# Optimization experiments

Measured on AMD Instinct MI355X. Metric: run time of the kernel, lower is better.

Reference implementation:

```python
import jax, jax.numpy as jnp
import numpy as np

B, N1, N2, F = 128, 100, 2000, 128
NC = N1 + N2
T = 10
L0, L1, L2 = 32, 32, 16


def setup_inputs() -> dict:
    key = jax.random.key(0)
    ks = jax.random.split(key, 16)
    atom_types = jnp.array([1, 6, 7, 8, 9, 11, 12, 15, 16, 17], dtype=jnp.int32)
    # per-type MLP params, stacked over type dim T (matches build():
    # stddev 1/sqrt(layer_size) for hidden layers, 0.01 for output, zero biases)
    inp = {
        "frag1_layer": jax.random.normal(ks[0], (B, N1, F), jnp.float32),
        "frag2_layer": jax.random.normal(ks[1], (B, N2, F), jnp.float32),
        "complex_layer": jax.random.normal(ks[2], (B, NC, F), jnp.float32),
        "frag1_z": jax.random.randint(ks[3], (B, N1), 0, 18, jnp.int32),
        "frag2_z": jax.random.randint(ks[4], (B, N2), 0, 18, jnp.int32),
        "complex_z": jax.random.randint(ks[5], (B, NC), 0, 18, jnp.int32),
        "type_w0": jax.random.normal(ks[6], (T, F, L0), jnp.float32) * (1.0 / np.sqrt(L0)),
        "type_b0": jnp.zeros((T, L0), jnp.float32),
        "type_w1": jax.random.normal(ks[7], (T, L0, L1), jnp.float32) * (1.0 / np.sqrt(L1)),
        "type_b1": jnp.zeros((T, L1), jnp.float32),
        "type_w2": jax.random.normal(ks[8], (T, L1, L2), jnp.float32) * (1.0 / np.sqrt(L2)),
        "type_b2": jnp.zeros((T, L2), jnp.float32),
        "out_w": jax.random.normal(ks[9], (T, L2, 1), jnp.float32) * 0.01,
        "out_b": jnp.zeros((T, 1), jnp.float32),
        "atom_types": atom_types,
    }
    return inp


def reference(frag1_layer, frag2_layer, complex_layer, frag1_z, frag2_z, complex_z,
              type_w0, type_b0, type_w1, type_b1, type_w2, type_b2,
              out_w, out_b, atom_types):
    def per_type_energy(x, z):
        # dense compute for ALL atom types, then mask-route (same math as original)
        h = jax.nn.relu(jnp.einsum('bnf,tfh->tbnh', x, type_w0) + type_b0[:, None, None, :])
        h = jax.nn.relu(jnp.einsum('tbnh,thk->tbnk', h, type_w1) + type_b1[:, None, None, :])
        h = jax.nn.relu(jnp.einsum('tbnk,tkm->tbnm', h, type_w2) + type_b2[:, None, None, :])
        o = jnp.einsum('tbnm,tmo->tbno', h, out_w)[..., 0] + out_b[:, None, None, 0]  # [T,B,N]
        mask = z[None, :, :] == atom_types[:, None, None]  # [T,B,N]
        per_atom = jnp.sum(jnp.where(mask, o, jnp.zeros_like(o)), axis=0)  # [B,N]
        return jnp.sum(per_atom, axis=1)  # [B]

    e1 = per_type_energy(frag1_layer, frag1_z)
    e2 = per_type_energy(frag2_layer, frag2_z)
    ec = per_type_energy(complex_layer, complex_z)
    binding = ec - (e1 + e2)
    return binding[:, None]  # [B,1]
```

## Files before the change

kernel.cpp:

```cpp
#include <hip/hip_runtime.h>

#define B_ 128
#define N1_ 100
#define N2_ 2000
#define NC_ 2100
#define F_ 128
#define NT_ 10
#define L0_ 32
#define L1_ 32
#define L2_ 16

#define NA1 (B_*N1_)
#define NA2 (B_*N2_)
#define NAC (B_*NC_)
#define NATOT (NA1+NA2+NAC)
#define NBUCK (NT_*B_)
#define CAP_B 512
#define NFILL (NATOT/256)

#define WT_STRIDEH 11520

#define WS_CURSORS 0
#define WS_WPACK   8192
#define WS_LISTS   (WS_WPACK + NT_*WT_STRIDEH*2)
#define WS_NEEDED  ((size_t)WS_LISTS + (size_t)NBUCK*CAP_B*4)

typedef short bf16x8 __attribute__((ext_vector_type(8)));
typedef float f32x4 __attribute__((ext_vector_type(4)));

#define MFMA(a,b,c) __builtin_amdgcn_mfma_f32_16x16x32_bf16((a),(b),(c),0,0,0)

__device__ __forceinline__ unsigned short f2bf(float f){
  unsigned u = __float_as_uint(f);
  unsigned r = (u + 0x7FFFu + ((u >> 16) & 1u)) >> 16;
  return (unsigned short)r;
}
__device__ __forceinline__ float bf2f(unsigned short h){
  return __uint_as_float(((unsigned)h) << 16);
}

__device__ __forceinline__ void cvt8u(uint4 a, uint4 b, bf16x8& hi, bf16x8& lo){
  unsigned u[8] = {a.x, a.y, a.z, a.w, b.x, b.y, b.z, b.w};
  union { bf16x8 v; unsigned uu[4]; } H, L;
  #pragma unroll
  for (int i = 0; i < 4; ++i){
    unsigned p = u[2*i], qq = u[2*i+1];
    H.uu[i] = __builtin_amdgcn_perm(qq, p, 0x07060302u);
    unsigned ra = __float_as_uint(__uint_as_float(p)  - __uint_as_float(p  & 0xFFFF0000u));
    unsigned rb = __float_as_uint(__uint_as_float(qq) - __uint_as_float(qq & 0xFFFF0000u));
    L.uu[i] = __builtin_amdgcn_perm(rb, ra, 0x07060302u);
  }
  hi = H.v; lo = L.v;
}

__device__ __forceinline__ unsigned packsplit(float h){
  unsigned uh = __float_as_uint(h);
  unsigned tr = uh & 0xFFFF0000u;
  float res = h - __uint_as_float(tr);
  return tr | (__float_as_uint(res) >> 16);
}

__device__ __forceinline__ void unpack8(uint4 p0, uint4 p1, bf16x8& hi, bf16x8& lo){
  unsigned pp[8] = {p0.x, p0.y, p0.z, p0.w, p1.x, p1.y, p1.z, p1.w};
  union { bf16x8 v; unsigned uu[4]; } H, L;
  #pragma unroll
  for (int i = 0; i < 4; ++i){
    H.uu[i] = __builtin_amdgcn_perm(pp[2*i+1], pp[2*i], 0x07060302u);
    L.uu[i] = __builtin_amdgcn_perm(pp[2*i+1], pp[2*i], 0x05040100u);
  }
  hi = H.v; lo = L.v;
}

__device__ __forceinline__ void decode_atom(int g,
    const int* __restrict__ z1, const int* __restrict__ z2, const int* __restrict__ zc,
    int& tensor, int& row, int& b, int& z){
  if (g < NA1){ tensor = 0; row = g; b = g / N1_; z = z1[g]; }
  else if (g < NA1 + NA2){ int i = g - NA1; tensor = 1; row = i; b = i / N2_; z = z2[i]; }
  else { int i = g - NA1 - NA2; tensor = 2; row = i; b = i / NC_; z = zc[i]; }
}


__global__ __launch_bounds__(256) void k_fillprep(
    const int* __restrict__ z1, const int* __restrict__ z2, const int* __restrict__ zc,
    const int* __restrict__ atypes,
    const float* __restrict__ tw0, const float* __restrict__ tb0,
    const float* __restrict__ tw1, const float* __restrict__ tb1,
    const float* __restrict__ tw2, const float* __restrict__ tb2,
    const float* __restrict__ ow, const float* __restrict__ ob,
    unsigned* __restrict__ cursors, unsigned* __restrict__ lists,
    unsigned short* __restrict__ wpack, float* __restrict__ out){
  int tid = threadIdx.x;
  if (blockIdx.x >= NFILL){
    int t = blockIdx.x - NFILL;
    unsigned short* base = wpack + (size_t)t * WT_STRIDEH;
    const float* w0 = tw0 + (size_t)t * (F_ * L0_);
    for (int i = tid; i < 4096; i += 256){
      int ks = i >> 10, rem = i & 1023;
      int nt = rem >> 9, rem2 = rem & 511;
      int lane = rem2 >> 3, e = rem2 & 7;
      float f = w0[(ks * 32 + (lane >> 4) * 8 + e) * L0_ + nt * 16 + (lane & 15)];
      unsigned short hi = f2bf(f);
      unsigned short lo = f2bf(f - bf2f(hi));
      int off = (ks * 2 + nt) * 1024 + lane * 8 + e;
      base[off] = hi;
      base[off + 512] = lo;
    }
    const float* w1 = tw1 + (size_t)t * (L0_ * L1_);
    for (int i = tid; i < 1024; i += 256){
      int nt = i >> 9, rem2 = i & 511;
      int lane = rem2 >> 3, e = rem2 & 7;
      float f = w1[((lane >> 4) * 8 + e) * L1_ + nt * 16 + (lane & 15)];
      unsigned short hi = f2bf(f);
      unsigned short lo = f2bf(f - bf2f(hi));
      int off = 8192 + nt * 1024 + lane * 8 + e;
      base[off] = hi;
      base[off + 512] = lo;
    }
    const float* w2 = tw2 + (size_t)t * (L1_ * L2_);
    for (int i = tid; i < 512; i += 256){
      int lane = i >> 3, e = i & 7;
      float f = w2[((lane >> 4) * 8 + e) * L2_ + (lane & 15)];
      unsigned short hi = f2bf(f);
      unsigned short lo = f2bf(f - bf2f(hi));
      int off = 10240 + lane * 8 + e;
      base[off] = hi;
      base[off + 512] = lo;
    }
    float* prm = (float*)(base + 11264);
    if (tid < 32) prm[tid] = tb0[t * L0_ + tid];
    else if (tid < 64) prm[tid] = tb1[t * L1_ + tid - 32];
    else if (tid < 80) prm[tid] = tb2[t * L2_ + tid - 64];
    else if (tid < 96) prm[tid] = ow[t * L2_ + tid - 80];
    else if (tid == 96) prm[96] = ob[t];
    if (t == 0 && tid >= 128 && tid < 128 + B_) out[tid - 128] = 0.0f;
    return;
  }
  __shared__ int lut[32];
  __shared__ unsigned lhist[NBUCK];
  __shared__ unsigned lbase[NBUCK];
  for (int i = tid; i < NBUCK; i += 256) lhist[i] = 0u;
  if (tid < 32) lut[tid] = -1;
  __syncthreads();
  if (tid < NT_) lut[atypes[tid] & 31] = tid;
  __syncthreads();
  int g = blockIdx.x * 256 + tid;
  int bucket = -1; unsigned entv = 0u;
  {
    int tensor, row, b, z;
    decode_atom(g, z1, z2, zc, tensor, row, b, z);
    int t = lut[z & 31];
    if (t >= 0){
      bucket = t * B_ + b;
      entv = (unsigned)row | ((unsigned)tensor << 19);
      atomicAdd(&lhist[bucket], 1u);
    }
  }
  __syncthreads();
  for (int i = tid; i < NBUCK; i += 256){
    unsigned c = lhist[i];
    lbase[i] = c ? atomicAdd(&cursors[i], c) : 0u;
    lhist[i] = 0u;
  }
  __syncthreads();
  if (bucket >= 0){
    unsigned rank = atomicAdd(&lhist[bucket], 1u) + lbase[bucket];
    if (rank < CAP_B) lists[(size_t)bucket * CAP_B + rank] = entv;
  }
}


__global__ __launch_bounds__(64, 2) void k_main(
    const float* __restrict__ f1, const float* __restrict__ f2, const float* __restrict__ fc,
    const unsigned short* __restrict__ wpack,
    const unsigned* __restrict__ cursors, const unsigned* __restrict__ lists,
    float* __restrict__ out){
  int bucket = blockIdx.y;
  int count = (int)cursors[bucket];
  if (count > CAP_B) count = CAP_B;
  int quarter = (count + 3) >> 2;
  int lstart = blockIdx.x * quarter;
  int lend = lstart + quarter; if (lend > count) lend = count;
  int mycount = lend - lstart;
  if (mycount <= 0) return;
  int t = bucket >> 7, b = bucket & 127;
  int lane = threadIdx.x, q = lane >> 4, r16 = lane & 15;

  const unsigned* lst = lists + (size_t)bucket * CAP_B;

  const unsigned short* wp = wpack + (size_t)t * WT_STRIDEH;
  bf16x8 w0h[8], w0l[8];
  #pragma unroll
  for (int j = 0; j < 8; ++j){
    w0h[j] = *(const bf16x8*)(wp + j * 1024 + lane * 8);
    w0l[j] = *(const bf16x8*)(wp + j * 1024 + 512 + lane * 8);
  }
  bf16x8 w1h[2], w1l[2];
  #pragma unroll
  for (int j = 0; j < 2; ++j){
    w1h[j] = *(const bf16x8*)(wp + 8192 + j * 1024 + lane * 8);
    w1l[j] = *(const bf16x8*)(wp + 8192 + j * 1024 + 512 + lane * 8);
  }
  bf16x8 w2h = *(const bf16x8*)(wp + 10240 + lane * 8);
  bf16x8 w2l = *(const bf16x8*)(wp + 10240 + 512 + lane * 8);
  const float* prm = (const float*)(wp + 11264);
  float b00 = prm[r16],      b01 = prm[16 + r16];
  float b10 = prm[32 + r16], b11 = prm[48 + r16];
  float b2v = prm[64 + r16], owv = prm[80 + r16], obv = prm[96];

  __shared__ unsigned H0[16][44];
  __shared__ unsigned H1[16][44];

  int ntiles = (mycount + 15) >> 4;

  uint4 P0, P1, P2, P3, P4, P5, P6, P7;
  uint4 Q0, Q1, Q2, Q3, Q4, Q5, Q6, Q7;
  bf16x8 aH[4], aL[4];
  float vacc = 0.0f, ssum = 0.0f;

#define FETCHE(j_) lst[min(lstart + (j_) * 16 + r16, lend - 1)]
#define SIGNOF(e_, j_) ((((j_) * 16 + r16) < mycount) ? (((((e_) >> 19) & 3u) == 2u) ? 1.0f : -1.0f) : 0.0f)
#define LOADT(Ej, R0,R1,R2,R3,R4,R5,R6,R7) { \
    int row_ = (int)((Ej) & 0x7FFFFu); \
    int tn_  = (int)(((Ej) >> 19) & 3u); \
    const float* xr_ = ((tn_ == 0) ? f1 : (tn_ == 1) ? f2 : fc) + (size_t)row_ * F_ + q * 8; \
    R0 = *(const uint4*)(xr_);       R1 = *(const uint4*)(xr_ + 4); \
    R2 = *(const uint4*)(xr_ + 32);  R3 = *(const uint4*)(xr_ + 36); \
    R4 = *(const uint4*)(xr_ + 64);  R5 = *(const uint4*)(xr_ + 68); \
    R6 = *(const uint4*)(xr_ + 96);  R7 = *(const uint4*)(xr_ + 100); }

#define MLPBODY(SGc) { \
    f32x4 c00 = {b00, b00, b00, b00}; \
    f32x4 c01 = {b01, b01, b01, b01}; \
    _Pragma("unroll") \
    for (int ks = 0; ks < 4; ++ks){ \
      c00 = MFMA(aH[ks], w0h[2*ks],   c00); \
      c00 = MFMA(aL[ks], w0h[2*ks],   c00); \
      c00 = MFMA(aH[ks], w0l[2*ks],   c00); \
      c01 = MFMA(aH[ks], w0h[2*ks+1], c01); \
      c01 = MFMA(aL[ks], w0h[2*ks+1], c01); \
      c01 = MFMA(aH[ks], w0l[2*ks+1], c01); \
    } \
    _Pragma("unroll") \
    for (int reg = 0; reg < 4; ++reg){ \
      H0[4 * q + reg][r16]      = packsplit(fmaxf(c00[reg], 0.0f)); \
      H0[4 * q + reg][16 + r16] = packsplit(fmaxf(c01[reg], 0.0f)); \
    } \
    asm volatile("s_waitcnt lgkmcnt(0)" ::: "memory"); \
    __builtin_amdgcn_sched_barrier(0); \
    bf16x8 a1H, a1L; \
    { const unsigned* pr_ = &H0[r16][8 * q]; \
      unpack8(*(const uint4*)pr_, *(const uint4*)(pr_ + 4), a1H, a1L); } \
    f32x4 c10 = {b10, b10, b10, b10}; \
    f32x4 c11 = {b11, b11, b11, b11}; \
    c10 = MFMA(a1H, w1h[0], c10); \
    c10 = MFMA(a1L, w1h[0], c10); \
    c10 = MFMA(a1H, w1l[0], c10); \
    c11 = MFMA(a1H, w1h[1], c11); \
    c11 = MFMA(a1L, w1h[1], c11); \
    c11 = MFMA(a1H, w1l[1], c11); \
    _Pragma("unroll") \
    for (int reg = 0; reg < 4; ++reg){ \
      H1[4 * q + reg][r16]      = packsplit(fmaxf(c10[reg], 0.0f)); \
      H1[4 * q + reg][16 + r16] = packsplit(fmaxf(c11[reg], 0.0f)); \
    } \
    asm volatile("s_waitcnt lgkmcnt(0)" ::: "memory"); \
    __builtin_amdgcn_sched_barrier(0); \
    bf16x8 a2H, a2L; \
    { const unsigned* pr_ = &H1[r16][8 * q]; \
      unpack8(*(const uint4*)pr_, *(const uint4*)(pr_ + 4), a2H, a2L); } \
    f32x4 c2 = {b2v, b2v, b2v, b2v}; \
    c2 = MFMA(a2H, w2h, c2); \
    c2 = MFMA(a2L, w2h, c2); \
    c2 = MFMA(a2H, w2l, c2); \
    _Pragma("unroll") \
    for (int reg = 0; reg < 4; ++reg){ \
      float ov = fmaxf(c2[reg], 0.0f) * owv; \
      float sgm = __shfl((SGc), 4 * q + reg, 64); \
      vacc = fmaf(ov, sgm, vacc); \
    } \
    ssum += (SGc); }

  float sgP, sgQ;
  {
    unsigned e0 = FETCHE(0);
    LOADT(e0, P0, P1, P2, P3, P4, P5, P6, P7);
    sgP = SIGNOF(e0, 0);
  }
  if (ntiles > 1){
    unsigned e1 = FETCHE(1);
    LOADT(e1, Q0, Q1, Q2, Q3, Q4, Q5, Q6, Q7);
    sgQ = SIGNOF(e1, 1);
  } else sgQ = 0.0f;
  unsigned eN = (ntiles > 2) ? FETCHE(2) : 0u;
  unsigned eM = (ntiles > 3) ? FETCHE(3) : 0u;

  for (int it = 0; it < ntiles; it += 2){
    {
      float sgc = sgP;
      cvt8u(P0, P1, aH[0], aL[0]);
      cvt8u(P2, P3, aH[1], aL[1]);
      cvt8u(P4, P5, aH[2], aL[2]);
      cvt8u(P6, P7, aH[3], aL[3]);
      if (it + 2 < ntiles){
        LOADT(eN, P0, P1, P2, P3, P4, P5, P6, P7);
        sgP = SIGNOF(eN, it + 2);
        if (it + 4 < ntiles) eN = FETCHE(it + 4);
      }
      MLPBODY(sgc)
    }
    if (it + 1 >= ntiles) break;
    {
      float sgc = sgQ;
      cvt8u(Q0, Q1, aH[0], aL[0]);
      cvt8u(Q2, Q3, aH[1], aL[1]);
      cvt8u(Q4, Q5, aH[2], aL[2]);
      cvt8u(Q6, Q7, aH[3], aL[3]);
      if (it + 3 < ntiles){
        LOADT(eM, Q0, Q1, Q2, Q3, Q4, Q5, Q6, Q7);
        sgQ = SIGNOF(eM, it + 3);
        if (it + 5 < ntiles) eM = FETCHE(it + 5);
      }
      MLPBODY(sgc)
    }
  }
#undef FETCHE
#undef SIGNOF
#undef LOADT
#undef MLPBODY

  vacc = fmaf(0.25f * obv, ssum, vacc);
  #pragma unroll
  for (int m = 1; m < 64; m <<= 1) vacc += __shfl_xor(vacc, m, 64);
  if (lane == 0) atomicAdd(&out[b], vacc);
}


__global__ __launch_bounds__(256) void k_naive(
    const float* __restrict__ f1, const float* __restrict__ f2, const float* __restrict__ fc,
    const int* __restrict__ z1, const int* __restrict__ z2, const int* __restrict__ zc,
    const float* __restrict__ tw0, const float* __restrict__ tb0,
    const float* __restrict__ tw1, const float* __restrict__ tb1,
    const float* __restrict__ tw2, const float* __restrict__ tb2,
    const float* __restrict__ ow, const float* __restrict__ ob,
    const int* __restrict__ atypes, float* __restrict__ out){
  __shared__ int lut[32];
  int tid = threadIdx.x;
  if (tid < 32) lut[tid] = -1;
  __syncthreads();
  if (tid < NT_) lut[atypes[tid] & 31] = tid;
  __syncthreads();
  int g = blockIdx.x * 256 + tid;
  if (g >= NATOT) return;
  int tensor, row, b, z;
  decode_atom(g, z1, z2, zc, tensor, row, b, z);
  int t = lut[z & 31];
  if (t < 0) return;
  const float* x = ((tensor == 0) ? f1 : (tensor == 1) ? f2 : fc) + (size_t)row * F_;
  float h0[L0_];
  #pragma unroll
  for (int j = 0; j < L0_; ++j) h0[j] = tb0[t * L0_ + j];
  for (int k = 0; k < F_; ++k){
    float xx = x[k];
    const float* wr = tw0 + t * (F_ * L0_) + k * L0_;
    #pragma unroll
    for (int j = 0; j < L0_; ++j) h0[j] = fmaf(xx, wr[j], h0[j]);
  }
  #pragma unroll
  for (int j = 0; j < L0_; ++j) h0[j] = fmaxf(h0[j], 0.0f);
  float h1[L1_];
  #pragma unroll
  for (int j = 0; j < L1_; ++j) h1[j] = tb1[t * L1_ + j];
  for (int k = 0; k < L0_; ++k){
    float hh = h0[k];
    const float* wr = tw1 + t * (L1_ * L1_) + k * L1_;
    #pragma unroll
    for (int j = 0; j < L1_; ++j) h1[j] = fmaf(hh, wr[j], h1[j]);
  }
  #pragma unroll
  for (int j = 0; j < L1_; ++j) h1[j] = fmaxf(h1[j], 0.0f);
  float h2[L2_];
  #pragma unroll
  for (int m = 0; m < L2_; ++m) h2[m] = tb2[t * L2_ + m];
  for (int k = 0; k < L1_; ++k){
    float hh = h1[k];
    const float* wr = tw2 + t * (L1_ * L2_) + k * L2_;
    #pragma unroll
    for (int m = 0; m < L2_; ++m) h2[m] = fmaf(hh, wr[m], h2[m]);
  }
  float o = ob[t];
  #pragma unroll
  for (int m = 0; m < L2_; ++m) o += fmaxf(h2[m], 0.0f) * ow[t * L2_ + m];
  float sgn = (tensor == 2) ? 1.0f : -1.0f;
  atomicAdd(&out[b], sgn * o);
}

extern "C" void kernel_launch(void* const* d_in, const int* in_sizes, int n_in,
                              void* d_out, int out_size, void* d_ws, size_t ws_size,
                              hipStream_t stream){
  const float* f1  = (const float*)d_in[0];
  const float* f2  = (const float*)d_in[1];
  const float* fc  = (const float*)d_in[2];
  const int*   z1  = (const int*)d_in[3];
  const int*   z2  = (const int*)d_in[4];
  const int*   zc  = (const int*)d_in[5];
  const float* tw0 = (const float*)d_in[6];
  const float* tb0 = (const float*)d_in[7];
  const float* tw1 = (const float*)d_in[8];
  const float* tb1 = (const float*)d_in[9];
  const float* tw2 = (const float*)d_in[10];
  const float* tb2 = (const float*)d_in[11];
  const float* ow  = (const float*)d_in[12];
  const float* ob  = (const float*)d_in[13];
  const int* atypes = (const int*)d_in[14];
  float* out = (float*)d_out;

  if (ws_size < WS_NEEDED){
    hipMemsetAsync(d_out, 0, B_ * sizeof(float), stream);
    k_naive<<<(NATOT + 255) / 256, 256, 0, stream>>>(
        f1, f2, fc, z1, z2, zc, tw0, tb0, tw1, tb1, tw2, tb2, ow, ob, atypes, out);
    return;
  }

  unsigned* cursors = (unsigned*)((char*)d_ws + WS_CURSORS);
  unsigned short* wpack = (unsigned short*)((char*)d_ws + WS_WPACK);
  unsigned* lists   = (unsigned*)((char*)d_ws + WS_LISTS);

  hipMemsetAsync(cursors, 0, NBUCK * sizeof(unsigned), stream);
  k_fillprep<<<NFILL + NT_, 256, 0, stream>>>(z1, z2, zc, atypes,
      tw0, tb0, tw1, tb1, tw2, tb2, ow, ob, cursors, lists, wpack, out);
  k_main<<<dim3(4, NBUCK), 64, 0, stream>>>(f1, f2, fc, wpack, cursors, lists, out);
}
```

Before: 59.02 us.

## Deepen input prefetch to three tiles and move W0 low-half weights to LDS

Adds a third register-resident prefetch buffer so the per-bucket loop runs with three atom tiles in flight instead of two, to hide more global-load latency. To free the registers this needs, the low-precision half of the first-layer weights moves from registers into shared memory and is reloaded from LDS on every MFMA step. The trade is extra LDS traffic and possible lgkmcnt stalls against the deeper memory pipeline, plus a risk of register spills.

```diff
diff --git a/kernel.cpp b/kernel.cpp
--- a/kernel.cpp
+++ b/kernel.cpp
@@ -186,14 +186,22 @@
   int lane = threadIdx.x, q = lane >> 4, r16 = lane & 15;
 
   const unsigned* lst = lists + (size_t)bucket * CAP_B;
-
   const unsigned short* wp = wpack + (size_t)t * WT_STRIDEH;
-  bf16x8 w0h[8], w0l[8];
+
+  __shared__ unsigned short W0L[4096];
+  __shared__ unsigned H0[16][44];
+  __shared__ unsigned H1[16][44];
+
   #pragma unroll
   for (int j = 0; j < 8; ++j){
+    uint4 v = *(const uint4*)(wp + j * 1024 + 512 + lane * 8);
+    *(uint4*)((unsigned char*)W0L + j * 1024 + lane * 16) = v;
+  }
+
+  bf16x8 w0h[8];
+  #pragma unroll
+  for (int j = 0; j < 8; ++j)
     w0h[j] = *(const bf16x8*)(wp + j * 1024 + lane * 8);
-    w0l[j] = *(const bf16x8*)(wp + j * 1024 + 512 + lane * 8);
-  }
   bf16x8 w1h[2], w1l[2];
   #pragma unroll
   for (int j = 0; j < 2; ++j){
@@ -207,38 +215,38 @@
   float b10 = prm[32 + r16], b11 = prm[48 + r16];
   float b2v = prm[64 + r16], owv = prm[80 + r16], obv = prm[96];
 
-  __shared__ unsigned H0[16][44];
-  __shared__ unsigned H1[16][44];
-
   int ntiles = (mycount + 15) >> 4;
 
   uint4 P0, P1, P2, P3, P4, P5, P6, P7;
   uint4 Q0, Q1, Q2, Q3, Q4, Q5, Q6, Q7;
+  uint4 R0, R1, R2, R3, R4, R5, R6, R7;
   bf16x8 aH[4], aL[4];
   float vacc = 0.0f, ssum = 0.0f;
 
 #define FETCHE(j_) lst[min(lstart + (j_) * 16 + r16, lend - 1)]
 #define SIGNOF(e_, j_) ((((j_) * 16 + r16) < mycount) ? (((((e_) >> 19) & 3u) == 2u) ? 1.0f : -1.0f) : 0.0f)
-#define LOADT(Ej, R0,R1,R2,R3,R4,R5,R6,R7) { \
+#define LOADT(Ej, T0,T1,T2,T3,T4,T5,T6,T7) { \
     int row_ = (int)((Ej) & 0x7FFFFu); \
     int tn_  = (int)(((Ej) >> 19) & 3u); \
     const float* xr_ = ((tn_ == 0) ? f1 : (tn_ == 1) ? f2 : fc) + (size_t)row_ * F_ + q * 8; \
-    R0 = *(const uint4*)(xr_);       R1 = *(const uint4*)(xr_ + 4); \
-    R2 = *(const uint4*)(xr_ + 32);  R3 = *(const uint4*)(xr_ + 36); \
-    R4 = *(const uint4*)(xr_ + 64);  R5 = *(const uint4*)(xr_ + 68); \
-    R6 = *(const uint4*)(xr_ + 96);  R7 = *(const uint4*)(xr_ + 100); }
+    T0 = *(const uint4*)(xr_);       T1 = *(const uint4*)(xr_ + 4); \
+    T2 = *(const uint4*)(xr_ + 32);  T3 = *(const uint4*)(xr_ + 36); \
+    T4 = *(const uint4*)(xr_ + 64);  T5 = *(const uint4*)(xr_ + 68); \
+    T6 = *(const uint4*)(xr_ + 96);  T7 = *(const uint4*)(xr_ + 100); }
 
 #define MLPBODY(SGc) { \
     f32x4 c00 = {b00, b00, b00, b00}; \
     f32x4 c01 = {b01, b01, b01, b01}; \
     _Pragma("unroll") \
     for (int ks = 0; ks < 4; ++ks){ \
+      bf16x8 wla = *(const bf16x8*)(W0L + (2*ks) * 512 + lane * 8); \
+      bf16x8 wlb = *(const bf16x8*)(W0L + (2*ks+1) * 512 + lane * 8); \
       c00 = MFMA(aH[ks], w0h[2*ks],   c00); \
       c00 = MFMA(aL[ks], w0h[2*ks],   c00); \
-      c00 = MFMA(aH[ks], w0l[2*ks],   c00); \
+      c00 = MFMA(aH[ks], wla,         c00); \
       c01 = MFMA(aH[ks], w0h[2*ks+1], c01); \
       c01 = MFMA(aL[ks], w0h[2*ks+1], c01); \
-      c01 = MFMA(aH[ks], w0l[2*ks+1], c01); \
+      c01 = MFMA(aH[ks], wlb,         c01); \
     } \
     _Pragma("unroll") \
     for (int reg = 0; reg < 4; ++reg){ \
@@ -280,7 +288,7 @@
     } \
     ssum += (SGc); }
 
-  float sgP, sgQ;
+  float sgP = 0.0f, sgQ = 0.0f, sgR = 0.0f;
   {
     unsigned e0 = FETCHE(0);
     LOADT(e0, P0, P1, P2, P3, P4, P5, P6, P7);
@@ -290,21 +298,27 @@
     unsigned e1 = FETCHE(1);
     LOADT(e1, Q0, Q1, Q2, Q3, Q4, Q5, Q6, Q7);
     sgQ = SIGNOF(e1, 1);
-  } else sgQ = 0.0f;
-  unsigned eN = (ntiles > 2) ? FETCHE(2) : 0u;
-  unsigned eM = (ntiles > 3) ? FETCHE(3) : 0u;
-
-  for (int it = 0; it < ntiles; it += 2){
+  }
+  if (ntiles > 2){
+    unsigned e2 = FETCHE(2);
+    LOADT(e2, R0, R1, R2, R3, R4, R5, R6, R7);
+    sgR = SIGNOF(e2, 2);
+  }
+  unsigned eN = (ntiles > 3) ? FETCHE(3) : 0u;
+  unsigned eM = (ntiles > 4) ? FETCHE(4) : 0u;
+  unsigned eO = (ntiles > 5) ? FETCHE(5) : 0u;
+
+  for (int it = 0; it < ntiles; it += 3){
     {
       float sgc = sgP;
       cvt8u(P0, P1, aH[0], aL[0]);
       cvt8u(P2, P3, aH[1], aL[1]);
       cvt8u(P4, P5, aH[2], aL[2]);
       cvt8u(P6, P7, aH[3], aL[3]);
-      if (it + 2 < ntiles){
+      if (it + 3 < ntiles){
         LOADT(eN, P0, P1, P2, P3, P4, P5, P6, P7);
-        sgP = SIGNOF(eN, it + 2);
-        if (it + 4 < ntiles) eN = FETCHE(it + 4);
+        sgP = SIGNOF(eN, it + 3);
+        if (it + 6 < ntiles) eN = FETCHE(it + 6);
       }
       MLPBODY(sgc)
     }
@@ -315,10 +329,24 @@
       cvt8u(Q2, Q3, aH[1], aL[1]);
       cvt8u(Q4, Q5, aH[2], aL[2]);
       cvt8u(Q6, Q7, aH[3], aL[3]);
-      if (it + 3 < ntiles){
+      if (it + 4 < ntiles){
         LOADT(eM, Q0, Q1, Q2, Q3, Q4, Q5, Q6, Q7);
-        sgQ = SIGNOF(eM, it + 3);
-        if (it + 5 < ntiles) eM = FETCHE(it + 5);
+        sgQ = SIGNOF(eM, it + 4);
+        if (it + 7 < ntiles) eM = FETCHE(it + 7);
+      }
+      MLPBODY(sgc)
+    }
+    if (it + 2 >= ntiles) break;
+    {
+      float sgc = sgR;
+      cvt8u(R0, R1, aH[0], aL[0]);
+      cvt8u(R2, R3, aH[1], aL[1]);
+      cvt8u(R4, R5, aH[2], aL[2]);
+      cvt8u(R6, R7, aH[3], aL[3]);
+      if (it + 5 < ntiles){
+        LOADT(eO, R0, R1, R2, R3, R4, R5, R6, R7);
+        sgR = SIGNOF(eO, it + 5);
+        if (it + 8 < ntiles) eO = FETCHE(it + 8);
       }
       MLPBODY(sgc)
     }
```

Result: slower. 60.51 us (+2.5%).
